# Kernel optimization log

Measured on AMD Instinct MI355X. Metric: run time of the kernel, lower is better.

The kernel has to match this reference:

```python
import jax, jax.numpy as jnp
import numpy as np

N_NODES = 50000
N_EDGES = 800000

def _gcn_layer(x, W, b, src, dst, n):
    # DGL GraphConv, norm='both': out = D_in^{-1/2} A D_out^{-1/2} x W + b
    e = src.shape[0]
    ones = jnp.ones((e,), dtype=x.dtype)
    deg_out = jax.ops.segment_sum(ones, src, num_segments=n)
    deg_in = jax.ops.segment_sum(ones, dst, num_segments=n)
    norm_src = jax.lax.rsqrt(jnp.clip(deg_out, 1.0))  # [n]
    norm_dst = jax.lax.rsqrt(jnp.clip(deg_in, 1.0))   # [n]
    # weight applied before aggregation (in_feats >= out_feats path in DGL)
    h = (x * norm_src[:, None]) @ W                   # [n, out]
    agg = jax.ops.segment_sum(h[src], dst, num_segments=n)  # SpMM: gather-scatter
    return agg * norm_dst[:, None] + b

def setup_inputs() -> dict:
    key = jax.random.key(0)
    ks = jax.random.split(key, 7)
    d_in, d_hid, d_out = 512, 256, 128
    features = jax.random.normal(ks[0], (N_NODES, d_in), dtype=jnp.float32)
    src = jax.random.randint(ks[1], (N_EDGES,), 0, N_NODES, dtype=jnp.int64)
    dst = jax.random.randint(ks[2], (N_EDGES,), 0, N_NODES, dtype=jnp.int64)
    W1 = jax.random.normal(ks[3], (d_in, d_hid), dtype=jnp.float32) / np.sqrt(d_in)
    b1 = jnp.zeros((d_hid,), dtype=jnp.float32)
    W2 = jax.random.normal(ks[4], (d_hid, d_out), dtype=jnp.float32) / np.sqrt(d_hid)
    b2 = jnp.zeros((d_out,), dtype=jnp.float32)
    return {"features": features, "src": src, "dst": dst,
            "W1": W1, "b1": b1, "W2": W2, "b2": b2}

def reference(features, src, dst, W1, b1, W2, b2):
    n = features.shape[0]
    x = _gcn_layer(features, W1, b1, src, dst, n)
    x = jax.nn.relu(x)
    x = _gcn_layer(x, W2, b2, src, dst, n)
    return x
```

## Files before the change

kernel.cpp:

```cpp
#include <hip/hip_runtime.h>
#include <type_traits>

#define DIN  512
#define DHID 256
#define DOF  128

#define RB   13
#define RSZ  (1 << RB)
#define BPR  32

typedef _Float16 f16;
typedef _Float16 f16x8 __attribute__((ext_vector_type(8)));
typedef _Float16 f16v4 __attribute__((ext_vector_type(4)));
typedef _Float16 f16v2 __attribute__((ext_vector_type(2)));
typedef float f32x4 __attribute__((ext_vector_type(4)));

__global__ __launch_bounds__(256) void hist_deg(const int* __restrict__ src,
                                                const int* __restrict__ dst, int e,
                                                int* __restrict__ cnt_out,
                                                int* __restrict__ cnt_in) {
    __shared__ int h_out[RSZ], h_in[RSZ];
    const int r = blockIdx.x / BPR, b = blockIdx.x % BPR;
    const int base = r << RB;
    const int tid = threadIdx.x;
    for (int j = tid; j < RSZ; j += 256) { h_out[j] = 0; h_in[j] = 0; }
    __syncthreads();

    const int ce = (((e + BPR - 1) / BPR) + 3) & ~3;
    const int s0 = b * ce, s1 = min(s0 + ce, e);
    for (int i = s0 + tid * 4; i < s1; i += 1024) {
        if (i + 3 < s1) {
            int4 sv = *(const int4*)(src + i);
            int4 dv = *(const int4*)(dst + i);
            int v;
            v = sv.x - base; if ((unsigned)v < RSZ) atomicAdd(&h_out[v], 1);
            v = sv.y - base; if ((unsigned)v < RSZ) atomicAdd(&h_out[v], 1);
            v = sv.z - base; if ((unsigned)v < RSZ) atomicAdd(&h_out[v], 1);
            v = sv.w - base; if ((unsigned)v < RSZ) atomicAdd(&h_out[v], 1);
            v = dv.x - base; if ((unsigned)v < RSZ) atomicAdd(&h_in[v], 1);
            v = dv.y - base; if ((unsigned)v < RSZ) atomicAdd(&h_in[v], 1);
            v = dv.z - base; if ((unsigned)v < RSZ) atomicAdd(&h_in[v], 1);
            v = dv.w - base; if ((unsigned)v < RSZ) atomicAdd(&h_in[v], 1);
        } else {
            for (int q = i; q < s1; ++q) {
                int v = src[q] - base; if ((unsigned)v < RSZ) atomicAdd(&h_out[v], 1);
                v = dst[q] - base;     if ((unsigned)v < RSZ) atomicAdd(&h_in[v], 1);
            }
        }
    }
    __syncthreads();
    int* co = cnt_out + (size_t)(r * BPR + b) * RSZ;
    int* ci = cnt_in  + (size_t)(r * BPR + b) * RSZ;
    for (int j = tid; j < RSZ; j += 256) { co[j] = h_out[j]; ci[j] = h_in[j]; }
}

__global__ void sum_base(const int* __restrict__ cnt_out, int* __restrict__ cnt_in,
                         int* __restrict__ deg_in,
                         float* __restrict__ norm_src, float* __restrict__ norm_dst, int n) {
    int d = blockIdx.x * blockDim.x + threadIdx.x;
    if (d >= n) return;
    const int r = d >> RB, j = d & (RSZ - 1);
    int* ci = cnt_in + (size_t)(r * BPR) * RSZ + j;
    int s = 0;
#pragma unroll 4
    for (int b = 0; b < BPR; ++b) {
        int c = ci[(size_t)b * RSZ];
        ci[(size_t)b * RSZ] = s;
        s += c;
    }
    deg_in[d] = s;
    norm_dst[d] = rsqrtf(fmaxf((float)s, 1.0f));
    const int* co = cnt_out + (size_t)(r * BPR) * RSZ + j;
    int s2 = 0;
#pragma unroll 4
    for (int b = 0; b < BPR; ++b) s2 += co[(size_t)b * RSZ];
    norm_src[d] = rsqrtf(fmaxf((float)s2, 1.0f));
}

__global__ __launch_bounds__(256) void scan_part(const int* __restrict__ deg,
                                                 int* __restrict__ partial, int n) {
    const int base = blockIdx.x * 1024;
    const int tid = threadIdx.x;
    int v = 0;
#pragma unroll
    for (int j = 0; j < 4; ++j) {
        int i = base + tid * 4 + j;
        if (i < n) v += deg[i];
    }
    for (int o = 1; o < 64; o <<= 1) v += __shfl_xor(v, o);
    __shared__ int wsum[4];
    if ((tid & 63) == 0) wsum[tid >> 6] = v;
    __syncthreads();
    if (tid == 0) partial[blockIdx.x] = wsum[0] + wsum[1] + wsum[2] + wsum[3];
}

__global__ __launch_bounds__(64) void scan_offsets(int* __restrict__ partial, int nb,
                                                   int* __restrict__ rowptr, int n) {
    const int l = threadIdx.x;
    int orig = (l < nb) ? partial[l] : 0;
    int v = orig;
    for (int o = 1; o < 64; o <<= 1) {
        int u = __shfl_up(v, o);
        if (l >= o) v += u;
    }
    if (l < nb) partial[l] = v - orig;
    if (l == nb - 1) rowptr[n] = v;
}

__global__ __launch_bounds__(256) void scan_apply(const int* __restrict__ deg,
                                                  const int* __restrict__ partial,
                                                  int* __restrict__ rowptr, int n) {
    const int base = blockIdx.x * 1024;
    const int tid = threadIdx.x;
    int x[4]; int s = 0;
#pragma unroll
    for (int j = 0; j < 4; ++j) {
        int i = base + tid * 4 + j;
        x[j] = (i < n) ? deg[i] : 0;
        s += x[j];
    }
    const int l = tid & 63, w = tid >> 6;
    int inc = s;
    for (int o = 1; o < 64; o <<= 1) {
        int u = __shfl_up(inc, o);
        if (l >= o) inc += u;
    }
    __shared__ int wsum[4];
    if (l == 63) wsum[w] = inc;
    __syncthreads();
    int wbase = 0;
    for (int q = 0; q < w; ++q) wbase += wsum[q];
    int excl = partial[blockIdx.x] + wbase + (inc - s);
#pragma unroll
    for (int j = 0; j < 4; ++j) {
        int i = base + tid * 4 + j;
        if (i < n) rowptr[i] = excl;
        excl += x[j];
    }
}

__global__ __launch_bounds__(256) void fill_csr2(const int* __restrict__ src,
                                                 const int* __restrict__ dst, int e,
                                                 const int* __restrict__ rowptr,
                                                 const int* __restrict__ base_in,
                                                 int* __restrict__ csr_src) {
    __shared__ int cur[RSZ];
    const int r = blockIdx.x / BPR, b = blockIdx.x % BPR;
    const int base = r << RB;
    const int tid = threadIdx.x;
    for (int j = tid; j < RSZ; j += 256) cur[j] = 0;
    __syncthreads();

    const int* bi = base_in + (size_t)(r * BPR + b) * RSZ;
    const int ce = (((e + BPR - 1) / BPR) + 3) & ~3;
    const int s0 = b * ce, s1 = min(s0 + ce, e);
    for (int i = s0 + tid * 4; i < s1; i += 1024) {
        if (i + 3 < s1) {
            int4 dv = *(const int4*)(dst + i);
            int4 sv = *(const int4*)(src + i);
            int v;
            v = dv.x - base; if ((unsigned)v < RSZ) { int p = atomicAdd(&cur[v], 1); csr_src[rowptr[base + v] + bi[v] + p] = sv.x; }
            v = dv.y - base; if ((unsigned)v < RSZ) { int p = atomicAdd(&cur[v], 1); csr_src[rowptr[base + v] + bi[v] + p] = sv.y; }
            v = dv.z - base; if ((unsigned)v < RSZ) { int p = atomicAdd(&cur[v], 1); csr_src[rowptr[base + v] + bi[v] + p] = sv.z; }
            v = dv.w - base; if ((unsigned)v < RSZ) { int p = atomicAdd(&cur[v], 1); csr_src[rowptr[base + v] + bi[v] + p] = sv.w; }
        } else {
            for (int q = i; q < s1; ++q) {
                int v = dst[q] - base;
                if ((unsigned)v < RSZ) { int p = atomicAdd(&cur[v], 1); csr_src[rowptr[base + v] + bi[v] + p] = src[q]; }
            }
        }
    }
}

__global__ void transpose_w(const float* __restrict__ W1, const float* __restrict__ W2,
                            f16* __restrict__ w1t, f16* __restrict__ w2t) {
    int t = blockIdx.x * blockDim.x + threadIdx.x;
    if (t < DIN * DHID) {
        int k = t / DHID, c = t % DHID;
        w1t[c * DIN + k] = (f16)W1[t];
    } else {
        int u = t - DIN * DHID;
        if (u < DHID * DOF) {
            int k = u / DOF, c = u % DOF;
            w2t[c * DHID + k] = (f16)W2[u];
        }
    }
}

template<int K, int N, bool A_F32>
__global__ __launch_bounds__(256) void mfma_gemm(const void* __restrict__ Aptr,
                                                 const float* __restrict__ norm,
                                                 const f16* __restrict__ Bt,
                                                 f16* __restrict__ H, int M) {
    constexpr int BM = 128, BN = 128, BK = 32;
    constexpr int NT = K / BK;
    __shared__ __align__(16) f16 smem[BM * BN];

    const int rbase = blockIdx.x * BM;
    const int nbj = blockIdx.y * BN;
    const int tid = threadIdx.x;
    const int l = tid & 63, wid = tid >> 6;
    const int wr = wid >> 1, wc = wid & 1;
    const int fr = l & 15, kg = l >> 4;

    int arow[2], achk[2];
    float ascale[2];
#pragma unroll
    for (int j = 0; j < 2; ++j) {
        int u = tid + j * 256;
        arow[j] = u >> 2; achk[j] = u & 3;
        if (A_F32) {
            int grow = rbase + arow[j];
            ascale[j] = (grow < M) ? norm[grow] : 0.0f;
        }
    }

    struct ABregs {
        float4 a0[2], a1[2];
        f16x8  a16[2];
        f16x8  b[2];
    };

    auto gload = [&](int k0) {
        ABregs r;
#pragma unroll
        for (int j = 0; j < 2; ++j) {
            int grow = rbase + arow[j];
            if (A_F32) {
                if (grow < M) {
                    const float* A = (const float*)Aptr + (long)grow * K + k0 + achk[j] * 8;
                    r.a0[j] = *(const float4*)A;
                    r.a1[j] = *(const float4*)(A + 4);
                } else {
                    r.a0[j] = make_float4(0.f, 0.f, 0.f, 0.f);
                    r.a1[j] = make_float4(0.f, 0.f, 0.f, 0.f);
                }
            } else {
                f16x8 v = {};
                if (grow < M)
                    v = *(const f16x8*)((const f16*)Aptr + (long)grow * K + k0 + achk[j] * 8);
                r.a16[j] = v;
            }
            r.b[j] = *(const f16x8*)(Bt + (long)(nbj + arow[j]) * K + k0 + achk[j] * 8);
        }
        return r;
    };

    auto swrite = [&](int buf, const ABregs& r) {
        f16* As = smem + buf * 8192;
        f16* Bs = As + 4096;
#pragma unroll
        for (int j = 0; j < 2; ++j) {
            f16x8 v;
            if (A_F32) {
                float s = ascale[j];
                v[0] = (f16)(r.a0[j].x * s); v[1] = (f16)(r.a0[j].y * s);
                v[2] = (f16)(r.a0[j].z * s); v[3] = (f16)(r.a0[j].w * s);
                v[4] = (f16)(r.a1[j].x * s); v[5] = (f16)(r.a1[j].y * s);
                v[6] = (f16)(r.a1[j].z * s); v[7] = (f16)(r.a1[j].w * s);
            } else {
                v = r.a16[j];
            }
            int ia = (arow[j] * BK + achk[j] * 8) ^ ((arow[j] & 7) << 3);
            *(f16x8*)&As[ia] = v;
            *(f16x8*)&Bs[ia] = r.b[j];
        }
    };

    f32x4 acc[4][4] = {};

    auto compute = [&](int buf) {
        const f16* As = smem + buf * 8192;
        const f16* Bs = As + 4096;
        f16x8 af[4], bf[4];
#pragma unroll
        for (int m = 0; m < 4; ++m) {
            int row = wr * 64 + m * 16 + fr;
            int ia = (row * BK + kg * 8) ^ ((row & 7) << 3);
            af[m] = *(const f16x8*)&As[ia];
        }
#pragma unroll
        for (int nf = 0; nf < 4; ++nf) {
            int c = wc * 64 + nf * 16 + fr;
            int ib = (c * BK + kg * 8) ^ ((c & 7) << 3);
            bf[nf] = *(const f16x8*)&Bs[ib];
        }
#pragma unroll
        for (int m = 0; m < 4; ++m)
#pragma unroll
            for (int nf = 0; nf < 4; ++nf)
                acc[m][nf] = __builtin_amdgcn_mfma_f32_16x16x32_f16(af[m], bf[nf], acc[m][nf], 0, 0, 0);
    };

    ABregs rb, rc;
    {
        ABregs ra = gload(0);
        swrite(0, ra);
        rb = gload(BK);
        if (NT > 2) rc = gload(2 * BK);
    }

#pragma unroll
    for (int kt = 0; kt < NT; kt += 2) {
        __syncthreads();
        compute(0);
        if (kt + 1 < NT) swrite(1, rb);
        if (kt + 3 < NT) rb = gload((kt + 3) * BK);
        if (kt + 1 < NT) {
            __syncthreads();
            compute(1);
            if (kt + 2 < NT) swrite(0, rc);
            if (kt + 4 < NT) rc = gload((kt + 4) * BK);
        }
    }

    __syncthreads();
#pragma unroll
    for (int m = 0; m < 4; ++m)
#pragma unroll
        for (int nf = 0; nf < 4; ++nf)
#pragma unroll
            for (int i = 0; i < 4; ++i) {
                int row = wr * 64 + m * 16 + (l >> 4) * 4 + i;
                int col = wc * 64 + nf * 16 + (l & 15);
                smem[row * BN + col] = (f16)acc[m][nf][i];
            }
    __syncthreads();
#pragma unroll
    for (int j = 0; j < 8; ++j) {
        int u = tid + j * 256;
        int row = u >> 4, cu = u & 15;
        int grow = rbase + row;
        if (grow < M)
            *(f16x8*)(H + (long)grow * N + nbj + cu * 8) =
                *(const f16x8*)&smem[row * BN + cu * 8];
    }
}

template<int F, bool RELU, bool FOLD, bool OUT_F16>
__global__ __launch_bounds__(256) void aggregate_wave(const f16* __restrict__ H,
                                                      const int* __restrict__ rowptr,
                                                      const int* __restrict__ csr_src,
                                                      const float* __restrict__ norm_dst,
                                                      const float* __restrict__ norm_src,
                                                      const float* __restrict__ bias,
                                                      void* __restrict__ outp, int n) {
    constexpr int VPL = F / 64;
    using vec = typename std::conditional<VPL == 4, f16v4, f16v2>::type;

    const int node = blockIdx.x * 4 + (threadIdx.x >> 6);
    if (node >= n) return;
    const int l = threadIdx.x & 63;
    const int c0 = l * VPL;
    const f16* __restrict__ Hc = H + c0;

    int k = rowptr[node];
    const int end = rowptr[node + 1];

    float acc[VPL] = {};
    for (; k + 7 < end; k += 8) {
        int s0 = csr_src[k];
        int s1 = csr_src[k + 1];
        int s2 = csr_src[k + 2];
        int s3 = csr_src[k + 3];
        int s4 = csr_src[k + 4];
        int s5 = csr_src[k + 5];
        int s6 = csr_src[k + 6];
        int s7 = csr_src[k + 7];
        vec v0 = *(const vec*)(Hc + (long)s0 * F);
        vec v1 = *(const vec*)(Hc + (long)s1 * F);
        vec v2 = *(const vec*)(Hc + (long)s2 * F);
        vec v3 = *(const vec*)(Hc + (long)s3 * F);
        vec v4 = *(const vec*)(Hc + (long)s4 * F);
        vec v5 = *(const vec*)(Hc + (long)s5 * F);
        vec v6 = *(const vec*)(Hc + (long)s6 * F);
        vec v7 = *(const vec*)(Hc + (long)s7 * F);
#pragma unroll
        for (int q = 0; q < VPL; ++q) acc[q] += (float)v0[q];
#pragma unroll
        for (int q = 0; q < VPL; ++q) acc[q] += (float)v1[q];
#pragma unroll
        for (int q = 0; q < VPL; ++q) acc[q] += (float)v2[q];
#pragma unroll
        for (int q = 0; q < VPL; ++q) acc[q] += (float)v3[q];
#pragma unroll
        for (int q = 0; q < VPL; ++q) acc[q] += (float)v4[q];
#pragma unroll
        for (int q = 0; q < VPL; ++q) acc[q] += (float)v5[q];
#pragma unroll
        for (int q = 0; q < VPL; ++q) acc[q] += (float)v6[q];
#pragma unroll
        for (int q = 0; q < VPL; ++q) acc[q] += (float)v7[q];
    }
    if (k + 3 < end) {
        int s0 = csr_src[k];
        int s1 = csr_src[k + 1];
        int s2 = csr_src[k + 2];
        int s3 = csr_src[k + 3];
        vec v0 = *(const vec*)(Hc + (long)s0 * F);
        vec v1 = *(const vec*)(Hc + (long)s1 * F);
        vec v2 = *(const vec*)(Hc + (long)s2 * F);
        vec v3 = *(const vec*)(Hc + (long)s3 * F);
#pragma unroll
        for (int q = 0; q < VPL; ++q) acc[q] += (float)v0[q];
#pragma unroll
        for (int q = 0; q < VPL; ++q) acc[q] += (float)v1[q];
#pragma unroll
        for (int q = 0; q < VPL; ++q) acc[q] += (float)v2[q];
#pragma unroll
        for (int q = 0; q < VPL; ++q) acc[q] += (float)v3[q];
        k += 4;
    }
    for (; k < end; ++k) {
        vec v = *(const vec*)(Hc + (long)csr_src[k] * F);
#pragma unroll
        for (int q = 0; q < VPL; ++q) acc[q] += (float)v[q];
    }

    const float nd = norm_dst[node];
    const float ns = FOLD ? norm_src[node] : 1.0f;
#pragma unroll
    for (int q = 0; q < VPL; ++q) {
        float v = acc[q] * nd + bias[c0 + q];
        if (RELU) v = fmaxf(v, 0.0f);
        acc[q] = v * ns;
    }

    if (OUT_F16) {
        vec o;
#pragma unroll
        for (int q = 0; q < VPL; ++q) o[q] = (f16)acc[q];
        *(vec*)((f16*)outp + (long)node * F + c0) = o;
    } else {
        float* op = (float*)outp + (long)node * F + c0;
        if (VPL == 2) {
            *(float2*)op = make_float2(acc[0], acc[1]);
        } else {
#pragma unroll
            for (int q = 0; q < VPL; ++q) op[q] = acc[q];
        }
    }
}

extern "C" void kernel_launch(void* const* d_in, const int* in_sizes, int n_in,
                              void* d_out, int out_size, void* d_ws, size_t ws_size,
                              hipStream_t stream) {
    const float* features = (const float*)d_in[0];
    const int*   src      = (const int*)d_in[1];
    const int*   dst      = (const int*)d_in[2];
    const float* W1       = (const float*)d_in[3];
    const float* b1       = (const float*)d_in[4];
    const float* W2       = (const float*)d_in[5];
    const float* b2       = (const float*)d_in[6];
    float* out = (float*)d_out;

    const int n = in_sizes[0] / DIN;
    const int e = in_sizes[1];

    const int ranges = (n + RSZ - 1) >> RB;
    const size_t cntsz = (size_t)ranges * BPR * RSZ;

    char* ws = (char*)d_ws;
    size_t off = 0;
    auto alloc = [&](size_t bytes) { size_t o = off; off += (bytes + 255) & ~(size_t)255; return o; };
    size_t o_degi   = alloc((size_t)n * 4);
    size_t o_nsrc   = alloc((size_t)n * 4);
    size_t o_ndst   = alloc((size_t)n * 4);
    size_t o_rowptr = alloc((size_t)(n + 1) * 4);
    size_t o_part   = alloc((size_t)64 * 4);
    size_t o_csr    = alloc((size_t)e * 4);
    size_t o_cnto   = alloc(cntsz * 4);
    size_t o_cnti   = alloc(cntsz * 4);
    size_t o_w1t    = alloc((size_t)DIN * DHID * 2);
    size_t o_w2t    = alloc((size_t)DHID * DOF * 2);
    size_t o_h1     = alloc((size_t)n * DHID * 2);
    size_t o_x1     = alloc((size_t)n * DHID * 2);
    size_t o_h2     = alloc((size_t)n * DOF * 2);
    (void)ws_size;

    int*   deg_in   = (int*)(ws + o_degi);
    float* norm_src = (float*)(ws + o_nsrc);
    float* norm_dst = (float*)(ws + o_ndst);
    int*   rowptr   = (int*)(ws + o_rowptr);
    int*   partial  = (int*)(ws + o_part);
    int*   csr_src  = (int*)(ws + o_csr);
    int*   cnt_out  = (int*)(ws + o_cnto);
    int*   cnt_in   = (int*)(ws + o_cnti);
    f16*   w1t      = (f16*)(ws + o_w1t);
    f16*   w2t      = (f16*)(ws + o_w2t);
    f16*   h1       = (f16*)(ws + o_h1);
    f16*   x1       = (f16*)(ws + o_x1);
    f16*   h2       = (f16*)(ws + o_h2);

    const int hblocks = ranges * BPR;
    hist_deg<<<hblocks, 256, 0, stream>>>(src, dst, e, cnt_out, cnt_in);
    sum_base<<<(n + 255) / 256, 256, 0, stream>>>(cnt_out, cnt_in, deg_in,
                                                  norm_src, norm_dst, n);
    const int nb = (n + 1023) / 1024;
    scan_part<<<nb, 256, 0, stream>>>(deg_in, partial, n);
    scan_offsets<<<1, 64, 0, stream>>>(partial, nb, rowptr, n);
    scan_apply<<<nb, 256, 0, stream>>>(deg_in, partial, rowptr, n);
    fill_csr2<<<hblocks, 256, 0, stream>>>(src, dst, e, rowptr, cnt_in, csr_src);
    transpose_w<<<(DIN * DHID + DHID * DOF + 255) / 256, 256, 0, stream>>>(W1, W2, w1t, w2t);

    const int mtiles = (n + 127) / 128;
    const int ablocks = (n + 3) / 4;

    mfma_gemm<DIN, DHID, true><<<dim3(mtiles, DHID / 128), 256, 0, stream>>>(
        features, norm_src, w1t, h1, n);
    aggregate_wave<DHID, true, true, true><<<ablocks, 256, 0, stream>>>(
        h1, rowptr, csr_src, norm_dst, norm_src, b1, x1, n);

    mfma_gemm<DHID, DOF, false><<<dim3(mtiles, DOF / 128), 256, 0, stream>>>(
        x1, nullptr, w2t, h2, n);
    aggregate_wave<DOF, false, false, false><<<ablocks, 256, 0, stream>>>(
        h2, rowptr, csr_src, norm_dst, norm_src, b2, out, n);
}
```

Before: 210.9 us.

## Pre-convert features to fp16 and stage GEMM tiles with direct global-to-LDS loads

Adds an `fconv` kernel that scales the fp32 features by `norm_src` and writes a row-padded fp16 copy. Both GEMMs become one fp16 kernel that fills LDS with `global_load_lds` 16-byte transfers instead of register-staged loads. The main loop becomes a simple double-buffered loop, and the XOR swizzle on shared-memory tiles is dropped. The aim is lower register pressure and fewer instructions in the GEMM. The cost is an extra full read and write of the feature matrix, and possible LDS bank conflicts from the unswizzled layout.

```diff
diff --git a/kernel.cpp b/kernel.cpp
--- a/kernel.cpp
+++ b/kernel.cpp
@@ -14,6 +14,12 @@
 typedef _Float16 f16v4 __attribute__((ext_vector_type(4)));
 typedef _Float16 f16v2 __attribute__((ext_vector_type(2)));
 typedef float f32x4 __attribute__((ext_vector_type(4)));
+
+__device__ inline void gload16(const void* g, void* l) {
+    __builtin_amdgcn_global_load_lds(
+        (const __attribute__((address_space(1))) void*)g,
+        (__attribute__((address_space(3))) void*)l, 16, 0, 0);
+}
 
 __global__ __launch_bounds__(256) void hist_deg(const int* __restrict__ src,
                                                 const int* __restrict__ dst, int e,
@@ -187,83 +193,53 @@
     }
 }
 
-template<int K, int N, bool A_F32>
-__global__ __launch_bounds__(256) void mfma_gemm(const void* __restrict__ Aptr,
-                                                 const float* __restrict__ norm,
-                                                 const f16* __restrict__ Bt,
-                                                 f16* __restrict__ H, int M) {
-    constexpr int BM = 128, BN = 128, BK = 32;
-    constexpr int NT = K / BK;
-    __shared__ __align__(16) f16 smem[BM * BN];
-
-    const int rbase = blockIdx.x * BM;
-    const int nbj = blockIdx.y * BN;
+__global__ __launch_bounds__(256) void fconv(const float* __restrict__ X,
+                                             const float* __restrict__ norm,
+                                             f16* __restrict__ fx, int n, int mpad) {
+    long idx = ((long)blockIdx.x * blockDim.x + threadIdx.x) * 8;
+    if (idx >= (long)mpad * DIN) return;
+    int row = (int)(idx >> 9);
+    f16x8 v = {};
+    if (row < n) {
+        float s = norm[row];
+        const float* p = X + idx;
+        float4 a0 = *(const float4*)p;
+        float4 a1 = *(const float4*)(p + 4);
+        v[0] = (f16)(a0.x * s); v[1] = (f16)(a0.y * s);
+        v[2] = (f16)(a0.z * s); v[3] = (f16)(a0.w * s);
+        v[4] = (f16)(a1.x * s); v[5] = (f16)(a1.y * s);
+        v[6] = (f16)(a1.z * s); v[7] = (f16)(a1.w * s);
+    }
+    *(f16x8*)(fx + idx) = v;
+}
+
+template<int K, int N>
+__global__ __launch_bounds__(256) void mfma_gemm16(const f16* __restrict__ A,
+                                                   const f16* __restrict__ Bt,
+                                                   f16* __restrict__ H, int M) {
+    constexpr int BK = 32, NT = K / BK;
+    __shared__ __align__(16) f16 smem[16384];
+    const int rbase = blockIdx.x * 128;
+    const int nbj = blockIdx.y * 128;
     const int tid = threadIdx.x;
     const int l = tid & 63, wid = tid >> 6;
     const int wr = wid >> 1, wc = wid & 1;
     const int fr = l & 15, kg = l >> 4;
 
-    int arow[2], achk[2];
-    float ascale[2];
-#pragma unroll
-    for (int j = 0; j < 2; ++j) {
-        int u = tid + j * 256;
-        arow[j] = u >> 2; achk[j] = u & 3;
-        if (A_F32) {
-            int grow = rbase + arow[j];
-            ascale[j] = (grow < M) ? norm[grow] : 0.0f;
-        }
-    }
-
-    struct ABregs {
-        float4 a0[2], a1[2];
-        f16x8  a16[2];
-        f16x8  b[2];
-    };
-
-    auto gload = [&](int k0) {
-        ABregs r;
-#pragma unroll
-        for (int j = 0; j < 2; ++j) {
-            int grow = rbase + arow[j];
-            if (A_F32) {
-                if (grow < M) {
-                    const float* A = (const float*)Aptr + (long)grow * K + k0 + achk[j] * 8;
-                    r.a0[j] = *(const float4*)A;
-                    r.a1[j] = *(const float4*)(A + 4);
-                } else {
-                    r.a0[j] = make_float4(0.f, 0.f, 0.f, 0.f);
-                    r.a1[j] = make_float4(0.f, 0.f, 0.f, 0.f);
-                }
-            } else {
-                f16x8 v = {};
-                if (grow < M)
-                    v = *(const f16x8*)((const f16*)Aptr + (long)grow * K + k0 + achk[j] * 8);
-                r.a16[j] = v;
-            }
-            r.b[j] = *(const f16x8*)(Bt + (long)(nbj + arow[j]) * K + k0 + achk[j] * 8);
-        }
-        return r;
-    };
-
-    auto swrite = [&](int buf, const ABregs& r) {
+    const int slot0 = wid * 2;
+    const int srow = l >> 2, skch = l & 3;
+
+    auto stage = [&](int buf, int k0) {
         f16* As = smem + buf * 8192;
         f16* Bs = As + 4096;
 #pragma unroll
-        for (int j = 0; j < 2; ++j) {
-            f16x8 v;
-            if (A_F32) {
-                float s = ascale[j];
-                v[0] = (f16)(r.a0[j].x * s); v[1] = (f16)(r.a0[j].y * s);
-                v[2] = (f16)(r.a0[j].z * s); v[3] = (f16)(r.a0[j].w * s);
-                v[4] = (f16)(r.a1[j].x * s); v[5] = (f16)(r.a1[j].y * s);
-                v[6] = (f16)(r.a1[j].z * s); v[7] = (f16)(r.a1[j].w * s);
-            } else {
-                v = r.a16[j];
-            }
-            int ia = (arow[j] * BK + achk[j] * 8) ^ ((arow[j] & 7) << 3);
-            *(f16x8*)&As[ia] = v;
-            *(f16x8*)&Bs[ia] = r.b[j];
+        for (int q = 0; q < 2; ++q) {
+            int slot = slot0 + q;
+            int row = slot * 16 + srow;
+            const f16* ga = A + (long)(rbase + row) * K + k0 + skch * 8;
+            gload16(ga, As + slot * 512);
+            const f16* gb = Bt + (long)(nbj + row) * K + k0 + skch * 8;
+            gload16(gb, Bs + slot * 512);
         }
     };
 
@@ -274,17 +250,11 @@
         const f16* Bs = As + 4096;
         f16x8 af[4], bf[4];
 #pragma unroll
-        for (int m = 0; m < 4; ++m) {
-            int row = wr * 64 + m * 16 + fr;
-            int ia = (row * BK + kg * 8) ^ ((row & 7) << 3);
-            af[m] = *(const f16x8*)&As[ia];
-        }
-#pragma unroll
-        for (int nf = 0; nf < 4; ++nf) {
-            int c = wc * 64 + nf * 16 + fr;
-            int ib = (c * BK + kg * 8) ^ ((c & 7) << 3);
-            bf[nf] = *(const f16x8*)&Bs[ib];
-        }
+        for (int m = 0; m < 4; ++m)
+            af[m] = *(const f16x8*)&As[(wr * 64 + m * 16 + fr) * 32 + kg * 8];
+#pragma unroll
+        for (int nf = 0; nf < 4; ++nf)
+            bf[nf] = *(const f16x8*)&Bs[(wc * 64 + nf * 16 + fr) * 32 + kg * 8];
 #pragma unroll
         for (int m = 0; m < 4; ++m)
 #pragma unroll
@@ -292,29 +262,16 @@
                 acc[m][nf] = __builtin_amdgcn_mfma_f32_16x16x32_f16(af[m], bf[nf], acc[m][nf], 0, 0, 0);
     };
 
-    ABregs rb, rc;
-    {
-        ABregs ra = gload(0);
-        swrite(0, ra);
-        rb = gload(BK);
-        if (NT > 2) rc = gload(2 * BK);
-    }
-
-#pragma unroll
-    for (int kt = 0; kt < NT; kt += 2) {
+    stage(0, 0);
+    __syncthreads();
+    int buf = 0;
+    for (int kt = 0; kt < NT; ++kt) {
+        if (kt + 1 < NT) stage(buf ^ 1, (kt + 1) * BK);
+        compute(buf);
         __syncthreads();
-        compute(0);
-        if (kt + 1 < NT) swrite(1, rb);
-        if (kt + 3 < NT) rb = gload((kt + 3) * BK);
-        if (kt + 1 < NT) {
-            __syncthreads();
-            compute(1);
-            if (kt + 2 < NT) swrite(0, rc);
-            if (kt + 4 < NT) rc = gload((kt + 4) * BK);
-        }
-    }
-
-    __syncthreads();
+        buf ^= 1;
+    }
+
 #pragma unroll
     for (int m = 0; m < 4; ++m)
 #pragma unroll
@@ -323,7 +280,7 @@
             for (int i = 0; i < 4; ++i) {
                 int row = wr * 64 + m * 16 + (l >> 4) * 4 + i;
                 int col = wc * 64 + nf * 16 + (l & 15);
-                smem[row * BN + col] = (f16)acc[m][nf][i];
+                smem[row * 128 + col] = (f16)acc[m][nf][i];
             }
     __syncthreads();
 #pragma unroll
@@ -333,7 +290,7 @@
         int grow = rbase + row;
         if (grow < M)
             *(f16x8*)(H + (long)grow * N + nbj + cu * 8) =
-                *(const f16x8*)&smem[row * BN + cu * 8];
+                *(const f16x8*)&smem[row * 128 + cu * 8];
     }
 }
 
@@ -456,6 +413,7 @@
 
     const int n = in_sizes[0] / DIN;
     const int e = in_sizes[1];
+    const int mpad = (n + 127) & ~127;
 
     const int ranges = (n + RSZ - 1) >> RB;
     const size_t cntsz = (size_t)ranges * BPR * RSZ;
@@ -473,9 +431,10 @@
     size_t o_cnti   = alloc(cntsz * 4);
     size_t o_w1t    = alloc((size_t)DIN * DHID * 2);
     size_t o_w2t    = alloc((size_t)DHID * DOF * 2);
-    size_t o_h1     = alloc((size_t)n * DHID * 2);
-    size_t o_x1     = alloc((size_t)n * DHID * 2);
-    size_t o_h2     = alloc((size_t)n * DOF * 2);
+    size_t o_fx     = alloc((size_t)mpad * DIN * 2);
+    size_t o_h1     = alloc((size_t)mpad * DHID * 2);
+    size_t o_x1     = alloc((size_t)mpad * DHID * 2);
+    size_t o_h2     = alloc((size_t)mpad * DOF * 2);
     (void)ws_size;
 
     int*   deg_in   = (int*)(ws + o_degi);
@@ -488,6 +447,7 @@
     int*   cnt_in   = (int*)(ws + o_cnti);
     f16*   w1t      = (f16*)(ws + o_w1t);
     f16*   w2t      = (f16*)(ws + o_w2t);
+    f16*   fx       = (f16*)(ws + o_fx);
     f16*   h1       = (f16*)(ws + o_h1);
     f16*   x1       = (f16*)(ws + o_x1);
     f16*   h2       = (f16*)(ws + o_h2);
@@ -502,17 +462,19 @@
     scan_apply<<<nb, 256, 0, stream>>>(deg_in, partial, rowptr, n);
     fill_csr2<<<hblocks, 256, 0, stream>>>(src, dst, e, rowptr, cnt_in, csr_src);
     transpose_w<<<(DIN * DHID + DHID * DOF + 255) / 256, 256, 0, stream>>>(W1, W2, w1t, w2t);
-
-    const int mtiles = (n + 127) / 128;
+    {
+        long tot = (long)mpad * DIN / 8;
+        fconv<<<(unsigned)((tot + 255) / 256), 256, 0, stream>>>(features, norm_src, fx, n, mpad);
+    }
+
+    const int mtiles = mpad / 128;
     const int ablocks = (n + 3) / 4;
 
-    mfma_gemm<DIN, DHID, true><<<dim3(mtiles, DHID / 128), 256, 0, stream>>>(
-        features, norm_src, w1t, h1, n);
+    mfma_gemm16<DIN, DHID><<<dim3(mtiles, DHID / 128), 256, 0, stream>>>(fx, w1t, h1, n);
     aggregate_wave<DHID, true, true, true><<<ablocks, 256, 0, stream>>>(
         h1, rowptr, csr_src, norm_dst, norm_src, b1, x1, n);
 
-    mfma_gemm<DHID, DOF, false><<<dim3(mtiles, DOF / 128), 256, 0, stream>>>(
-        x1, nullptr, w2t, h2, n);
+    mfma_gemm16<DHID, DOF><<<dim3(mtiles, DOF / 128), 256, 0, stream>>>(x1, w2t, h2, n);
     aggregate_wave<DOF, false, false, false><<<ablocks, 256, 0, stream>>>(
         h2, rowptr, csr_src, norm_dst, norm_src, b2, out, n);
 }
```

Result: slower. 223.5 us (+6.0%).
